# Kernel tuning notes

Measured on AMD Instinct MI355X. Metric: run time of the kernel, lower is better.

The kernel has to match this reference:

```python
import jax, jax.numpy as jnp
import numpy as np

N_NODES = 50000
N_EDGES = 800000
IN_DIM = 256
HID = 32
HEADS = 8
OUT_DIM = 16
NEG_SLOPE = 0.2


def setup_inputs() -> dict:
    key = jax.random.key(0)
    ks = jax.random.split(key, 12)
    s = 0.05
    return {
        "emb": jax.random.normal(ks[0], (N_NODES, IN_DIM), jnp.float32),
        "src": jax.random.randint(ks[1], (N_EDGES,), 0, N_NODES),
        "dst": jax.random.randint(ks[2], (N_EDGES,), 0, N_NODES),
        "W1": jax.random.normal(ks[3], (IN_DIM, HEADS * HID), jnp.float32) * s,
        "attn_l1": jax.random.normal(ks[4], (HEADS, HID), jnp.float32) * s,
        "attn_r1": jax.random.normal(ks[5], (HEADS, HID), jnp.float32) * s,
        "bias1": jax.random.normal(ks[6], (HEADS * HID,), jnp.float32) * s,
        "W2": jax.random.normal(ks[7], (HEADS * HID, OUT_DIM), jnp.float32) * s,
        "attn_l2": jax.random.normal(ks[8], (1, OUT_DIM), jnp.float32) * s,
        "attn_r2": jax.random.normal(ks[9], (1, OUT_DIM), jnp.float32) * s,
        "bias2": jax.random.normal(ks[10], (OUT_DIM,), jnp.float32) * s,
    }


def gat_conv(x, src, dst, W, attn_l, attn_r, bias, n_heads, d_out):
    # x: [N, F_in] -> per-head projection h: [N, H, D]
    n = x.shape[0]
    h = (x @ W).reshape(n, n_heads, d_out)
    el = jnp.sum(h * attn_l, axis=-1)  # [N, H]
    er = jnp.sum(h * attn_r, axis=-1)  # [N, H]
    # edge scores with LeakyReLU (DGL negative_slope=0.2)
    e = jax.nn.leaky_relu(el[src] + er[dst], NEG_SLOPE)  # [E, H]
    # edge softmax over incoming edges of each destination node
    m = jax.ops.segment_max(e, dst, num_segments=n)  # [N, H]
    ee = jnp.exp(e - m[dst])
    denom = jax.ops.segment_sum(ee, dst, num_segments=n)  # [N, H]
    alpha = ee / denom[dst]  # [E, H]
    # weighted scatter-sum aggregation
    out = jax.ops.segment_sum(h[src] * alpha[:, :, None], dst, num_segments=n)  # [N, H, D]
    return out + bias.reshape(1, n_heads, d_out)


def reference(emb, src, dst, W1, attn_l1, attn_r1, bias1, W2, attn_l2, attn_r2, bias2):
    h = gat_conv(emb, src, dst, W1, attn_l1, attn_r1, bias1, HEADS, HID)  # [N, 8, 32]
    h = jax.nn.elu(h.reshape(N_NODES, HEADS * HID))  # [N, 256]
    out = gat_conv(h, src, dst, W2, attn_l2, attn_r2, bias2, 1, OUT_DIM)  # [N, 1, 16]
    return jnp.squeeze(out, axis=1)  # [N, 16]
```

## Files before the change

kernel.cpp:

```cpp
#include <hip/hip_runtime.h>
#include <math.h>

#define N_NODES 50000
#define N_EDGES 800000
#define NEG_SLOPE 0.2f

typedef __attribute__((ext_vector_type(8))) short bf16x8;
typedef __attribute__((ext_vector_type(4))) float f32x4;
typedef __attribute__((ext_vector_type(4))) _Float16 half4;

__device__ inline unsigned short f32_to_bf16_rn(float x) {
    unsigned u = __builtin_bit_cast(unsigned, x);
    unsigned r = u + 0x7fffu + ((u >> 16) & 1u);
    return (unsigned short)(r >> 16);
}
__device__ inline float bf16_bits_to_f32(unsigned short h) {
    unsigned u = ((unsigned)h) << 16;
    return __builtin_bit_cast(float, u);
}
__device__ inline void load_lds16(const void* g, void* l) {
    __builtin_amdgcn_global_load_lds(
        (const __attribute__((address_space(1))) void*)g,
        (__attribute__((address_space(3))) void*)l, 16, 0, 0);
}


__device__ __forceinline__ void count_body(int bb, const int* __restrict__ dst,
                                           int* __restrict__ deg) {
    int i = bb * 256 + threadIdx.x;
    if (i < N_EDGES) atomicAdd(&deg[dst[i]], 1);
}

__device__ __forceinline__ void convert_body(int n, const float* __restrict__ W,
                                             unsigned short* __restrict__ Th,
                                             unsigned short* __restrict__ Tl) {
    int k = threadIdx.x;
    float x = W[k * 256 + n];
    unsigned short h = f32_to_bf16_rn(x);
    float lo = x - bf16_bits_to_f32(h);
    size_t idx = ((size_t)(k >> 3) * 256 + n) * 8 + (k & 7);
    Th[idx] = h;
    Tl[idx] = f32_to_bf16_rn(lo);
}

__device__ __forceinline__ void assign_body(int bb, const int* __restrict__ deg,
                                            int* __restrict__ offs,
                                            int* __restrict__ cursor,
                                            int* __restrict__ gcounter) {
    __shared__ int buf[256];
    __shared__ int base;
    int tid = threadIdx.x;
    int v = bb * 256 + tid;
    int d = (v < N_NODES) ? deg[v] : 0;
    buf[tid] = d;
    __syncthreads();
    for (int off = 1; off < 256; off <<= 1) {
        int x = (tid >= off) ? buf[tid - off] : 0;
        __syncthreads();
        buf[tid] += x;
        __syncthreads();
    }
    if (tid == 255) base = atomicAdd(gcounter, buf[255]);
    __syncthreads();
    if (v < N_NODES) {
        int start = base + buf[tid] - d;
        offs[v] = start;
        cursor[v] = start;
    }
}

__device__ __forceinline__ void scatter_body(int bb, const int* __restrict__ src,
                                             const int* __restrict__ dst,
                                             int* __restrict__ cursor,
                                             int* __restrict__ src_csr) {
    int i = bb * 256 + threadIdx.x;
    if (i < N_EDGES) {
        int p = atomicAdd(&cursor[dst[i]], 1);
        src_csr[p] = src[i];
    }
}


__device__ __forceinline__ void gemm1_body(int bb, const float* __restrict__ A,
                                           const unsigned short* __restrict__ BTh,
                                           const unsigned short* __restrict__ BTl,
                                           const float* __restrict__ al,
                                           const float* __restrict__ ar,
                                           _Float16* __restrict__ C,
                                           float* __restrict__ el,
                                           float* __restrict__ er, int M) {
    __shared__ unsigned short Ah[4][64][8], Al[4][64][8];
    __shared__ unsigned short Bh[4][256][8], Bl[4][256][8];
    int tid = threadIdx.x;
    int lane = tid & 63, wave = tid >> 6;
    int kgl = lane >> 4, rl = lane & 15;
    int row0 = bb * 64;

    f32x4 acc[4][4];
#pragma unroll
    for (int i = 0; i < 4; i++)
#pragma unroll
        for (int j = 0; j < 4; j++) acc[i][j] = (f32x4){0.f, 0.f, 0.f, 0.f};

    int rowA = tid >> 2, kgA = tid & 3;
    int grA = row0 + rowA;
    const float* pA = &A[(size_t)grA * 256 + kgA * 8];
    float4 x0 = make_float4(0.f, 0.f, 0.f, 0.f);
    float4 x1 = make_float4(0.f, 0.f, 0.f, 0.f);
    if (grA < M) {
        x0 = *reinterpret_cast<const float4*>(pA);
        x1 = *reinterpret_cast<const float4*>(pA + 4);
    }

    for (int step = 0; step < 8; step++) {
        int k0 = step * 32;
        {
            float xs[8] = {x0.x, x0.y, x0.z, x0.w, x1.x, x1.y, x1.z, x1.w};
            unsigned short hs[8], ls[8];
#pragma unroll
            for (int j = 0; j < 8; j++) {
                hs[j] = f32_to_bf16_rn(xs[j]);
                ls[j] = f32_to_bf16_rn(xs[j] - bf16_bits_to_f32(hs[j]));
            }
            *reinterpret_cast<bf16x8*>(&Ah[kgA][rowA][0]) = *reinterpret_cast<bf16x8*>(hs);
            *reinterpret_cast<bf16x8*>(&Al[kgA][rowA][0]) = *reinterpret_cast<bf16x8*>(ls);
        }
        int s0 = k0 >> 3;
#pragma unroll
        for (int i = 0; i < 4; i++) {
            load_lds16(&BTh[((size_t)(s0 + i) * 256 + tid) * 8], &Bh[i][wave << 6][0]);
            load_lds16(&BTl[((size_t)(s0 + i) * 256 + tid) * 8], &Bl[i][wave << 6][0]);
        }
        __syncthreads();
        if (step < 7 && grA < M) {
            x0 = *reinterpret_cast<const float4*>(pA + (step + 1) * 32);
            x1 = *reinterpret_cast<const float4*>(pA + (step + 1) * 32 + 4);
        }
        bf16x8 a_h[4], a_l[4];
#pragma unroll
        for (int mf = 0; mf < 4; mf++) {
            int row = mf * 16 + rl;
            a_h[mf] = *reinterpret_cast<bf16x8*>(&Ah[kgl][row][0]);
            a_l[mf] = *reinterpret_cast<bf16x8*>(&Al[kgl][row][0]);
        }
#pragma unroll
        for (int nf = 0; nf < 4; nf++) {
            int col = wave * 64 + nf * 16 + rl;
            bf16x8 bh = *reinterpret_cast<bf16x8*>(&Bh[kgl][col][0]);
            bf16x8 bl = *reinterpret_cast<bf16x8*>(&Bl[kgl][col][0]);
#pragma unroll
            for (int mf = 0; mf < 4; mf++) {
                acc[mf][nf] = __builtin_amdgcn_mfma_f32_16x16x32_bf16(a_h[mf], bh, acc[mf][nf], 0, 0, 0);
                acc[mf][nf] = __builtin_amdgcn_mfma_f32_16x16x32_bf16(a_h[mf], bl, acc[mf][nf], 0, 0, 0);
                acc[mf][nf] = __builtin_amdgcn_mfma_f32_16x16x32_bf16(a_l[mf], bh, acc[mf][nf], 0, 0, 0);
            }
        }
        __syncthreads();
    }
    float alv[4], arv[4];
#pragma unroll
    for (int nf = 0; nf < 4; nf++) {
        int c = wave * 64 + nf * 16 + rl;
        alv[nf] = al[c];
        arv[nf] = ar[c];
    }
#pragma unroll
    for (int mf = 0; mf < 4; mf++) {
#pragma unroll
        for (int rr = 0; rr < 4; rr++) {
            int grow = row0 + mf * 16 + (lane >> 4) * 4 + rr;
            bool ok = grow < M;
            if (ok) {
#pragma unroll
                for (int nf = 0; nf < 4; nf++) {
                    int gcol = wave * 64 + nf * 16 + rl;
                    C[(size_t)grow * 256 + gcol] = (_Float16)acc[mf][nf][rr];
                }
            }
            float e0 = acc[mf][0][rr] * alv[0] + acc[mf][1][rr] * alv[1];
            float e1 = acc[mf][2][rr] * alv[2] + acc[mf][3][rr] * alv[3];
            float f0 = acc[mf][0][rr] * arv[0] + acc[mf][1][rr] * arv[1];
            float f1 = acc[mf][2][rr] * arv[2] + acc[mf][3][rr] * arv[3];
#pragma unroll
            for (int off = 8; off >= 1; off >>= 1) {
                e0 += __shfl_down(e0, off, 16);
                e1 += __shfl_down(e1, off, 16);
                f0 += __shfl_down(f0, off, 16);
                f1 += __shfl_down(f1, off, 16);
            }
            if (rl == 0 && ok) {
                int h0 = wave * 2;
                el[grow * 8 + h0] = e0;
                el[grow * 8 + h0 + 1] = e1;
                er[grow * 8 + h0] = f0;
                er[grow * 8 + h0 + 1] = f1;
            }
        }
    }
}


__global__ __launch_bounds__(256) void k_count_convert(const int* __restrict__ dst,
                                                       int* __restrict__ deg,
                                                       const float* __restrict__ W1,
                                                       unsigned short* __restrict__ Th,
                                                       unsigned short* __restrict__ Tl) {
    int b = blockIdx.x;
    if (b < 3125) count_body(b, dst, deg);
    else convert_body(b - 3125, W1, Th, Tl);
}

__global__ __launch_bounds__(256) void k_gemmA_assign(const float* __restrict__ A,
                                                      const unsigned short* __restrict__ BTh,
                                                      const unsigned short* __restrict__ BTl,
                                                      const float* __restrict__ al,
                                                      const float* __restrict__ ar,
                                                      _Float16* __restrict__ C,
                                                      float* __restrict__ el,
                                                      float* __restrict__ er, int M,
                                                      const int* __restrict__ deg,
                                                      int* __restrict__ offs,
                                                      int* __restrict__ cursor,
                                                      int* __restrict__ gcounter) {
    int b = blockIdx.x;
    if (b < 391) gemm1_body(b, A, BTh, BTl, al, ar, C, el, er, M);
    else assign_body(b - 391, deg, offs, cursor, gcounter);
}

__global__ __launch_bounds__(256) void k_gemmB_scatter(const float* __restrict__ A,
                                                       const unsigned short* __restrict__ BTh,
                                                       const unsigned short* __restrict__ BTl,
                                                       const float* __restrict__ al,
                                                       const float* __restrict__ ar,
                                                       _Float16* __restrict__ C,
                                                       float* __restrict__ el,
                                                       float* __restrict__ er, int M,
                                                       const int* __restrict__ src,
                                                       const int* __restrict__ dst,
                                                       int* __restrict__ cursor,
                                                       int* __restrict__ src_csr) {
    int b = blockIdx.x;
    if (b < 391) gemm1_body(391 + b, A, BTh, BTl, al, ar, C, el, er, M);
    else scatter_body(b - 391, src, dst, cursor, src_csr);
}


__global__ __launch_bounds__(64) void agg1_fused(const int* __restrict__ offs,
                                                 const int* __restrict__ deg_arr,
                                                 const int* __restrict__ src_csr,
                                                 const float* __restrict__ el,
                                                 const float* __restrict__ er,
                                                 const _Float16* __restrict__ h1h,
                                                 const float* __restrict__ bias1,
                                                 _Float16* __restrict__ x2) {
    __shared__ float sc[64][8];
    int v = blockIdx.x;
    int t = threadIdx.x;
    int head = t >> 3, slot = t & 7;
    int start = offs[v];
    int deg = deg_arr[v];
    int end = start + deg;
    int ncache = (deg < 64) ? deg : 64;
    float erv = er[v * 8 + head];
    float s = 0.f;
    for (int base = 0; base < ncache; base += 8) {
        int e = base + slot;
        if (e < ncache) {
            int u = src_csr[start + e];
            float x = el[u * 8 + head] + erv;
            x = (x >= 0.f) ? x : NEG_SLOPE * x;
            float ex = expf(x);
            sc[e][head] = ex;
            s += ex;
        }
    }
    for (int base = 64; base < deg; base += 8) {
        int e = base + slot;
        if (e < deg) {
            int u = src_csr[start + e];
            float x = el[u * 8 + head] + erv;
            x = (x >= 0.f) ? x : NEG_SLOPE * x;
            s += expf(x);
        }
    }
    s += __shfl_xor(s, 1);
    s += __shfl_xor(s, 2);
    s += __shfl_xor(s, 4);
    float invs = (s > 0.f) ? 1.f / s : 0.f;
    __syncthreads();
    float4 acc = make_float4(0.f, 0.f, 0.f, 0.f);
    int i = start;
    for (; i + 3 < end && (i - start) + 3 < 64; i += 4) {
        int e = i - start;
        int u0 = src_csr[i];
        int u1 = src_csr[i + 1];
        int u2 = src_csr[i + 2];
        int u3 = src_csr[i + 3];
        float a0 = sc[e][head] * invs;
        float a1 = sc[e + 1][head] * invs;
        float a2 = sc[e + 2][head] * invs;
        float a3 = sc[e + 3][head] * invs;
        half4 p0 = *reinterpret_cast<const half4*>(&h1h[(size_t)u0 * 256 + 4 * t]);
        half4 p1 = *reinterpret_cast<const half4*>(&h1h[(size_t)u1 * 256 + 4 * t]);
        half4 p2 = *reinterpret_cast<const half4*>(&h1h[(size_t)u2 * 256 + 4 * t]);
        half4 p3 = *reinterpret_cast<const half4*>(&h1h[(size_t)u3 * 256 + 4 * t]);
        acc.x += a0 * (float)p0[0] + a1 * (float)p1[0] + a2 * (float)p2[0] + a3 * (float)p3[0];
        acc.y += a0 * (float)p0[1] + a1 * (float)p1[1] + a2 * (float)p2[1] + a3 * (float)p3[1];
        acc.z += a0 * (float)p0[2] + a1 * (float)p1[2] + a2 * (float)p2[2] + a3 * (float)p3[2];
        acc.w += a0 * (float)p0[3] + a1 * (float)p1[3] + a2 * (float)p2[3] + a3 * (float)p3[3];
    }
    for (; i < end; i++) {
        int e = i - start;
        int u0 = src_csr[i];
        float a0;
        if (e < 64) {
            a0 = sc[e][head] * invs;
        } else {
            float x = el[u0 * 8 + head] + erv;
            x = (x >= 0.f) ? x : NEG_SLOPE * x;
            a0 = expf(x) * invs;
        }
        half4 p0 = *reinterpret_cast<const half4*>(&h1h[(size_t)u0 * 256 + 4 * t]);
        acc.x += a0 * (float)p0[0];
        acc.y += a0 * (float)p0[1];
        acc.z += a0 * (float)p0[2];
        acc.w += a0 * (float)p0[3];
    }
    float4 b = *reinterpret_cast<const float4*>(&bias1[4 * t]);
    float ox = acc.x + b.x, oy = acc.y + b.y, oz = acc.z + b.z, ow = acc.w + b.w;
    ox = (ox > 0.f) ? ox : (expf(ox) - 1.f);
    oy = (oy > 0.f) ? oy : (expf(oy) - 1.f);
    oz = (oz > 0.f) ? oz : (expf(oz) - 1.f);
    ow = (ow > 0.f) ? ow : (expf(ow) - 1.f);
    half4 o = {(_Float16)ox, (_Float16)oy, (_Float16)oz, (_Float16)ow};
    *reinterpret_cast<half4*>(&x2[(size_t)v * 256 + 4 * t]) = o;
}


__global__ __launch_bounds__(256) void gemm2_mfma(const _Float16* __restrict__ X,
                                                  const float* __restrict__ W2,
                                                  const float* __restrict__ al,
                                                  const float* __restrict__ ar,
                                                  float* __restrict__ h2,
                                                  float* __restrict__ el2,
                                                  float* __restrict__ er2, int M) {
    __shared__ unsigned short Xh[16][64][8], Xl[16][64][8];
    __shared__ unsigned short Wh[32][16][8], Wl[32][16][8];
    int tid = threadIdx.x;
    int lane = tid & 63, wave = tid >> 6;
    int kgl = lane >> 4, rl = lane & 15;
    int row0 = blockIdx.x * 64;

#pragma unroll
    for (int j = 0; j < 16; j++) {
        int e = tid * 16 + j;
        float x = W2[e];
        unsigned short h = f32_to_bf16_rn(x);
        unsigned short l = f32_to_bf16_rn(x - bf16_bits_to_f32(h));
        int k = e >> 4, c = e & 15;
        Wh[k >> 3][c][k & 7] = h;
        Wl[k >> 3][c][k & 7] = l;
    }

    f32x4 acc = (f32x4){0.f, 0.f, 0.f, 0.f};
    int rowX = tid >> 2, kgb = (tid & 3) * 4;
    int grX = row0 + rowX;
    for (int step = 0; step < 2; step++) {
#pragma unroll
        for (int j = 0; j < 4; j++) {
            int kg = kgb + j;
            int kglob = step * 128 + kg * 8;
            unsigned short hs[8], ls[8];
            if (grX < M) {
                half4 a0 = *reinterpret_cast<const half4*>(&X[(size_t)grX * 256 + kglob]);
                half4 a1 = *reinterpret_cast<const half4*>(&X[(size_t)grX * 256 + kglob + 4]);
                float xs[8] = {(float)a0[0], (float)a0[1], (float)a0[2], (float)a0[3],
                               (float)a1[0], (float)a1[1], (float)a1[2], (float)a1[3]};
#pragma unroll
                for (int q = 0; q < 8; q++) {
                    hs[q] = f32_to_bf16_rn(xs[q]);
                    ls[q] = f32_to_bf16_rn(xs[q] - bf16_bits_to_f32(hs[q]));
                }
            } else {
#pragma unroll
                for (int q = 0; q < 8; q++) { hs[q] = 0; ls[q] = 0; }
            }
            *reinterpret_cast<bf16x8*>(&Xh[kg][rowX][0]) = *reinterpret_cast<bf16x8*>(hs);
            *reinterpret_cast<bf16x8*>(&Xl[kg][rowX][0]) = *reinterpret_cast<bf16x8*>(ls);
        }
        __syncthreads();
#pragma unroll
        for (int ks = 0; ks < 4; ks++) {
            int kg = ks * 4 + kgl;
            int kgw = step * 16 + kg;
            bf16x8 a_h = *reinterpret_cast<bf16x8*>(&Xh[kg][wave * 16 + rl][0]);
            bf16x8 a_l = *reinterpret_cast<bf16x8*>(&Xl[kg][wave * 16 + rl][0]);
            bf16x8 b_h = *reinterpret_cast<bf16x8*>(&Wh[kgw][rl][0]);
            bf16x8 b_l = *reinterpret_cast<bf16x8*>(&Wl[kgw][rl][0]);
            acc = __builtin_amdgcn_mfma_f32_16x16x32_bf16(a_h, b_h, acc, 0, 0, 0);
            acc = __builtin_amdgcn_mfma_f32_16x16x32_bf16(a_h, b_l, acc, 0, 0, 0);
            acc = __builtin_amdgcn_mfma_f32_16x16x32_bf16(a_l, b_h, acc, 0, 0, 0);
        }
        __syncthreads();
    }
    float alv = al[rl], arv = ar[rl];
#pragma unroll
    for (int rr = 0; rr < 4; rr++) {
        int grow = row0 + wave * 16 + (lane >> 4) * 4 + rr;
        bool ok = grow < M;
        if (ok) h2[(size_t)grow * 16 + rl] = acc[rr];
        float pl = acc[rr] * alv;
        float pr = acc[rr] * arv;
#pragma unroll
        for (int off = 8; off >= 1; off >>= 1) {
            pl += __shfl_down(pl, off, 16);
            pr += __shfl_down(pr, off, 16);
        }
        if (rl == 0 && ok) {
            el2[grow] = pl;
            er2[grow] = pr;
        }
    }
}


__global__ __launch_bounds__(64) void agg2_fused(const int* __restrict__ offs,
                                                 const int* __restrict__ deg_arr,
                                                 const int* __restrict__ src_csr,
                                                 const float* __restrict__ el2,
                                                 const float* __restrict__ er2,
                                                 const float* __restrict__ h2,
                                                 const float* __restrict__ bias2,
                                                 float* __restrict__ out) {
    __shared__ float sc2[64];
    int v = blockIdx.x;
    int t = threadIdx.x;
    int start = offs[v];
    int deg = deg_arr[v];
    int end = start + deg;
    int ncache = (deg < 64) ? deg : 64;
    float erv = er2[v];
    float s = 0.f;
    for (int e = t; e < ncache; e += 64) {
        int u = src_csr[start + e];
        float x = el2[u] + erv;
        x = (x >= 0.f) ? x : NEG_SLOPE * x;
        float ex = expf(x);
        sc2[e] = ex;
        s += ex;
    }
    for (int e = 64 + t; e < deg; e += 64) {
        int u = src_csr[start + e];
        float x = el2[u] + erv;
        x = (x >= 0.f) ? x : NEG_SLOPE * x;
        s += expf(x);
    }
#pragma unroll
    for (int off = 32; off >= 1; off >>= 1) s += __shfl_xor(s, off);
    float invs = (s > 0.f) ? 1.f / s : 0.f;
    __syncthreads();
    int eg = t >> 4, d = t & 15;
    float acc = 0.f;
    for (int i = start + eg; i < end; i += 4) {
        int e = i - start;
        int u = src_csr[i];
        float a;
        if (e < 64) {
            a = sc2[e] * invs;
        } else {
            float x = el2[u] + erv;
            x = (x >= 0.f) ? x : NEG_SLOPE * x;
            a = expf(x) * invs;
        }
        acc += a * h2[(size_t)u * 16 + d];
    }
    acc += __shfl_xor(acc, 32);
    acc += __shfl_xor(acc, 16);
    if (t < 16) out[(size_t)v * 16 + t] = acc + bias2[t];
}


extern "C" void kernel_launch(void* const* d_in, const int* in_sizes, int n_in,
                              void* d_out, int out_size, void* d_ws, size_t ws_size,
                              hipStream_t stream) {
    const float* emb   = (const float*)d_in[0];
    const int*   src   = (const int*)d_in[1];
    const int*   dst   = (const int*)d_in[2];
    const float* W1    = (const float*)d_in[3];
    const float* al1   = (const float*)d_in[4];
    const float* ar1   = (const float*)d_in[5];
    const float* bias1 = (const float*)d_in[6];
    const float* W2    = (const float*)d_in[7];
    const float* al2   = (const float*)d_in[8];
    const float* ar2   = (const float*)d_in[9];
    const float* bias2 = (const float*)d_in[10];
    float* out = (float*)d_out;

    char* ws = (char*)d_ws;
    auto alloc = [&](size_t bytes) -> void* {
        void* p = ws;
        ws += (bytes + 255) & ~(size_t)255;
        return p;
    };
    int* deg     = (int*)alloc((N_NODES + 64) * 4);
    int* gcounter = deg + N_NODES;
    int* cursor  = (int*)alloc(N_NODES * 4);
    int* offs    = (int*)alloc(N_NODES * 4);
    int* src_csr = (int*)alloc(N_EDGES * 4);
    unsigned short* W1Th = (unsigned short*)alloc(256 * 256 * 2);
    unsigned short* W1Tl = (unsigned short*)alloc(256 * 256 * 2);
    _Float16* h1h = (_Float16*)alloc((size_t)N_NODES * 256 * 2);
    float* el1   = (float*)alloc(N_NODES * 8 * 4);
    float* er1   = (float*)alloc(N_NODES * 8 * 4);
    _Float16* x2h = (_Float16*)alloc((size_t)N_NODES * 256 * 2);
    float* h2    = (float*)alloc((size_t)N_NODES * 16 * 4);
    float* el2   = (float*)alloc(N_NODES * 4);
    float* er2   = (float*)alloc(N_NODES * 4);

    hipMemsetAsync(deg, 0, (N_NODES + 1) * 4, stream);
    k_count_convert<<<3381, 256, 0, stream>>>(dst, deg, W1, W1Th, W1Tl);
    k_gemmA_assign<<<587, 256, 0, stream>>>(emb, W1Th, W1Tl, al1, ar1, h1h, el1, er1,
                                            N_NODES, deg, offs, cursor, gcounter);
    k_gemmB_scatter<<<3516, 256, 0, stream>>>(emb, W1Th, W1Tl, al1, ar1, h1h, el1, er1,
                                              N_NODES, src, dst, cursor, src_csr);
    agg1_fused<<<N_NODES, 64, 0, stream>>>(offs, deg, src_csr, el1, er1, h1h, bias1, x2h);
    gemm2_mfma<<<(N_NODES + 63) / 64, 256, 0, stream>>>(x2h, W2, al2, ar2, h2, el2, er2, N_NODES);
    agg2_fused<<<N_NODES, 64, 0, stream>>>(offs, deg, src_csr, el2, er2, h2, bias2, out);
}
```

Measured before the change: 222.1 us.

## Unsplit gemm1 from scatter and store layer-2 features as fp16

New measurement: 239.7 us. +7.9%, slower.

```diff
diff --git a/kernel.cpp b/kernel.cpp
--- a/kernel.cpp
+++ b/kernel.cpp
@@ -69,11 +69,9 @@
     }
 }
 
-__device__ __forceinline__ void scatter_body(int bb, const int* __restrict__ src,
-                                             const int* __restrict__ dst,
-                                             int* __restrict__ cursor,
-                                             int* __restrict__ src_csr) {
-    int i = bb * 256 + threadIdx.x;
+__global__ void scatter_edges(const int* __restrict__ src, const int* __restrict__ dst,
+                              int* __restrict__ cursor, int* __restrict__ src_csr) {
+    int i = blockIdx.x * 256 + threadIdx.x;
     if (i < N_EDGES) {
         int p = atomicAdd(&cursor[dst[i]], 1);
         src_csr[p] = src[i];
@@ -210,7 +208,7 @@
     else convert_body(b - 3125, W1, Th, Tl);
 }
 
-__global__ __launch_bounds__(256) void k_gemmA_assign(const float* __restrict__ A,
+__global__ __launch_bounds__(256) void k_gemm1_assign(const float* __restrict__ A,
                                                       const unsigned short* __restrict__ BTh,
                                                       const unsigned short* __restrict__ BTl,
                                                       const float* __restrict__ al,
@@ -223,25 +221,8 @@
                                                       int* __restrict__ cursor,
                                                       int* __restrict__ gcounter) {
     int b = blockIdx.x;
-    if (b < 391) gemm1_body(b, A, BTh, BTl, al, ar, C, el, er, M);
-    else assign_body(b - 391, deg, offs, cursor, gcounter);
-}
-
-__global__ __launch_bounds__(256) void k_gemmB_scatter(const float* __restrict__ A,
-                                                       const unsigned short* __restrict__ BTh,
-                                                       const unsigned short* __restrict__ BTl,
-                                                       const float* __restrict__ al,
-                                                       const float* __restrict__ ar,
-                                                       _Float16* __restrict__ C,
-                                                       float* __restrict__ el,
-                                                       float* __restrict__ er, int M,
-                                                       const int* __restrict__ src,
-                                                       const int* __restrict__ dst,
-                                                       int* __restrict__ cursor,
-                                                       int* __restrict__ src_csr) {
-    int b = blockIdx.x;
-    if (b < 391) gemm1_body(391 + b, A, BTh, BTl, al, ar, C, el, er, M);
-    else scatter_body(b - 391, src, dst, cursor, src_csr);
+    if (b < 782) gemm1_body(b, A, BTh, BTl, al, ar, C, el, er, M);
+    else assign_body(b - 782, deg, offs, cursor, gcounter);
 }
 
 
@@ -341,7 +322,7 @@
                                                   const float* __restrict__ W2,
                                                   const float* __restrict__ al,
                                                   const float* __restrict__ ar,
-                                                  float* __restrict__ h2,
+                                                  _Float16* __restrict__ h2,
                                                   float* __restrict__ el2,
                                                   float* __restrict__ er2, int M) {
     __shared__ unsigned short Xh[16][64][8], Xl[16][64][8];
@@ -408,7 +389,7 @@
     for (int rr = 0; rr < 4; rr++) {
         int grow = row0 + wave * 16 + (lane >> 4) * 4 + rr;
         bool ok = grow < M;
-        if (ok) h2[(size_t)grow * 16 + rl] = acc[rr];
+        if (ok) h2[(size_t)grow * 16 + rl] = (_Float16)acc[rr];
         float pl = acc[rr] * alv;
         float pr = acc[rr] * arv;
 #pragma unroll
@@ -429,7 +410,7 @@
                                                  const int* __restrict__ src_csr,
                                                  const float* __restrict__ el2,
                                                  const float* __restrict__ er2,
-                                                 const float* __restrict__ h2,
+                                                 const _Float16* __restrict__ h2,
                                                  const float* __restrict__ bias2,
                                                  float* __restrict__ out) {
     __shared__ float sc2[64];
@@ -472,7 +453,7 @@
             x = (x >= 0.f) ? x : NEG_SLOPE * x;
             a = expf(x) * invs;
         }
-        acc += a * h2[(size_t)u * 16 + d];
+        acc += a * (float)h2[(size_t)u * 16 + d];
     }
     acc += __shfl_xor(acc, 32);
     acc += __shfl_xor(acc, 16);
@@ -513,17 +494,16 @@
     float* el1   = (float*)alloc(N_NODES * 8 * 4);
     float* er1   = (float*)alloc(N_NODES * 8 * 4);
     _Float16* x2h = (_Float16*)alloc((size_t)N_NODES * 256 * 2);
-    float* h2    = (float*)alloc((size_t)N_NODES * 16 * 4);
+    _Float16* h2h = (_Float16*)alloc((size_t)N_NODES * 16 * 2);
     float* el2   = (float*)alloc(N_NODES * 4);
     float* er2   = (float*)alloc(N_NODES * 4);
 
     hipMemsetAsync(deg, 0, (N_NODES + 1) * 4, stream);
     k_count_convert<<<3381, 256, 0, stream>>>(dst, deg, W1, W1Th, W1Tl);
-    k_gemmA_assign<<<587, 256, 0, stream>>>(emb, W1Th, W1Tl, al1, ar1, h1h, el1, er1,
+    k_gemm1_assign<<<978, 256, 0, stream>>>(emb, W1Th, W1Tl, al1, ar1, h1h, el1, er1,
                                             N_NODES, deg, offs, cursor, gcounter);
-    k_gemmB_scatter<<<3516, 256, 0, stream>>>(emb, W1Th, W1Tl, al1, ar1, h1h, el1, er1,
-                                              N_NODES, src, dst, cursor, src_csr);
+    scatter_edges<<<3125, 256, 0, stream>>>(src, dst, cursor, src_csr);
     agg1_fused<<<N_NODES, 64, 0, stream>>>(offs, deg, src_csr, el1, er1, h1h, bias1, x2h);
-    gemm2_mfma<<<(N_NODES + 63) / 64, 256, 0, stream>>>(x2h, W2, al2, ar2, h2, el2, er2, N_NODES);
-    agg2_fused<<<N_NODES, 64, 0, stream>>>(offs, deg, src_csr, el2, er2, h2, bias2, out);
-}
+    gemm2_mfma<<<(N_NODES + 63) / 64, 256, 0, stream>>>(x2h, W2, al2, ar2, h2h, el2, er2, N_NODES);
+    agg2_fused<<<N_NODES, 64, 0, stream>>>(offs, deg, src_csr, el2, er2, h2h, bias2, out);
+}
```
